# Optimization experiments

Measured on AMD Instinct MI355X. Metric: run time of the kernel, lower is better.

## Reference

```python
import jax, jax.numpy as jnp
import numpy as np

N = 8192
IN_F = 512
OUT_F = 64
NEG_INF = -9e15

def setup_inputs() -> dict:
    key = jax.random.key(0)
    k1, k2, k3, k4 = jax.random.split(key, 4)
    node_features = jax.random.normal(k1, (N, IN_F), dtype=jnp.float32)
    adjacency_matrix = jax.random.randint(k2, (N, N), 0, 2, dtype=jnp.int32)
    # Xavier-uniform-like init (gain 1.414), scale irrelevant for correctness
    w_bound = 1.414 * np.sqrt(6.0 / (IN_F + OUT_F))
    a_bound = 1.414 * np.sqrt(6.0 / (2 * OUT_F + 1))
    weight_matrix = jax.random.uniform(k3, (IN_F, OUT_F), minval=-w_bound, maxval=w_bound, dtype=jnp.float32)
    attention_vector = jax.random.uniform(k4, (2 * OUT_F, 1), minval=-a_bound, maxval=a_bound, dtype=jnp.float32)
    return {
        "node_features": node_features,
        "adjacency_matrix": adjacency_matrix,
        "weight_matrix": weight_matrix,
        "attention_vector": attention_vector,
    }

def reference(node_features, adjacency_matrix, weight_matrix, attention_vector):
    # h: [N, F] transformed features
    h = node_features @ weight_matrix
    # score[i, j] = h[i] . a_left + h[j] . a_right
    a_left = attention_vector[:OUT_F, 0]   # [F]
    a_right = attention_vector[OUT_F:, 0]  # [F]
    scores = (h @ a_left)[:, None] + (h @ a_right)[None, :]  # [N, N]
    # NOTE: source defines leaky_relu but never applies it in forward — faithful omission.
    masked = jnp.where(adjacency_matrix > 0, scores, NEG_INF)
    attn = jax.nn.softmax(masked, axis=1)  # [N, N]
    # dropout p=0 / inference: no-op
    out = attn @ h  # [N, F]
    return jax.nn.elu(out)  # concat=True path
```

## Files before the change

kernel.cpp:

```cpp
#include <hip/hip_runtime.h>
#include <hip/hip_bf16.h>
#include <cstdint>

#define NN      8192
#define OF      64
#define KC      16
#define CW      512
#define PSTR    65
#define RBYTES  1024

#define OFF_HW  0
#define OFF_P   1310720
#define OFF_BM  35389440

typedef __attribute__((ext_vector_type(8))) short  s16x8;
typedef __attribute__((ext_vector_type(4))) float  f32x4;

__device__ __forceinline__ unsigned short f2bf(float f) {
  unsigned int u = __float_as_uint(f);
  unsigned int r = (u + 0x7FFFu + ((u >> 16) & 1u)) >> 16;
  return (unsigned short)r;
}

__global__ __launch_bounds__(256) void ka_pack(const int* __restrict__ A,
                                               unsigned char* __restrict__ BM) {
  int t = threadIdx.x;
  int l = t & 63, w = t >> 6;
  int row = blockIdx.x * 4 + w;
  const int* ap = A + (size_t)row * NN + l * 8;
  unsigned char* bp = BM + (size_t)row * RBYTES + l;
#pragma unroll 4
  for (int i = 0; i < 16; ++i) {
    int4 a = *(const int4*)(ap + i * 512);
    int4 b = *(const int4*)(ap + i * 512 + 4);
    unsigned by = (unsigned)(a.x | (a.y << 1) | (a.z << 2) | (a.w << 3) |
                             (b.x << 4) | (b.y << 5) | (b.z << 6) | (b.w << 7));
    bp[i * 64] = (unsigned char)by;
  }
}

__global__ __launch_bounds__(256) void k1_hw(const float* __restrict__ X,
                                             const float* __restrict__ W,
                                             const float* __restrict__ att,
                                             unsigned short* __restrict__ HW) {
  __shared__ float xs[16 * 516];
  __shared__ float ws[64 * 68];
  int t = threadIdx.x;
  int rb = blockIdx.x * 16;

  {
    const float4* src = (const float4*)(X + (size_t)rb * 512);
#pragma unroll
    for (int s = 0; s < 8; ++s) {
      int lid = s * 256 + t;
      int row = lid >> 7, kseg = lid & 127;
      *(float4*)&xs[row * 516 + kseg * 4] = src[row * 128 + kseg];
    }
  }

  int row = t >> 4, tx = t & 15;
  float4 acc = {0.f, 0.f, 0.f, 0.f};
  for (int kc = 0; kc < 8; ++kc) {
    __syncthreads();
#pragma unroll
    for (int s = 0; s < 4; ++s) {
      int lid = s * 256 + t;
      int k = lid >> 4, cs = lid & 15;
      *(float4*)&ws[k * 68 + cs * 4] =
          *(const float4*)(W + (size_t)(kc * 64 + k) * 64 + cs * 4);
    }
    __syncthreads();
#pragma unroll 16
    for (int k = 0; k < 64; ++k) {
      float x = xs[row * 516 + kc * 64 + k];
      float4 w4 = *(const float4*)&ws[k * 68 + tx * 4];
      acc.x += x * w4.x; acc.y += x * w4.y;
      acc.z += x * w4.z; acc.w += x * w4.w;
    }
  }

  float v = acc.x * att[64 + tx * 4]     + acc.y * att[64 + tx * 4 + 1] +
            acc.z * att[64 + tx * 4 + 2] + acc.w * att[64 + tx * 4 + 3];
#pragma unroll
  for (int m = 8; m > 0; m >>= 1) v += __shfl_xor(v, m, 64);
  float e = expf(v);

  int j = rb + row;
  unsigned short* hw = HW + j;
  float hv[4] = {acc.x, acc.y, acc.z, acc.w};
#pragma unroll
  for (int c = 0; c < 4; ++c)
    hw[(size_t)(tx * 4 + c) * NN] = f2bf(e * hv[c]);
  if (tx == 0) hw[(size_t)64 * NN] = f2bf(e);
}

__device__ __forceinline__ s16x8 expand8(unsigned m) {
  union { unsigned u[4]; s16x8 v; } r;
#pragma unroll
  for (int j = 0; j < 4; ++j)
    r.u[j] = (((m >> (2 * j)) & 1u) | (((m >> (2 * j + 1)) & 1u) << 16)) * 0x3F80u;
  return r.v;
}

__device__ __forceinline__ unsigned u4c(uint4 v, int c) {
  return c == 0 ? v.x : c == 1 ? v.y : c == 2 ? v.z : v.w;
}

__global__ __launch_bounds__(256, 2) void k3_gat(const unsigned char* __restrict__ BM,
                                                 const unsigned short* __restrict__ HW,
                                                 float* __restrict__ P) {
  __shared__ unsigned short bt[65 * 512];

  int t = threadIdx.x;
  int kc = blockIdx.x & 15;
  int mg = blockIdx.x >> 4;
  int lane = t & 63, w = t >> 6;
  int l15 = lane & 15, q = lane >> 4;
  int k0 = kc * CW;
  int rowM = mg * 128;

  uint4 abits[2][4];
#pragma unroll
  for (int mt = 0; mt < 2; ++mt) {
    const uint4* p = (const uint4*)(BM +
        (size_t)(rowM + w * 32 + mt * 16 + l15) * RBYTES + kc * 64);
#pragma unroll
    for (int i = 0; i < 4; ++i) abits[mt][i] = p[i];
  }

#pragma unroll
  for (int rds = 0; rds < 16; ++rds) {
    int lid = rds * 256 + t;
    int row = lid >> 6, ch = lid & 63;
    uint4 v = *(const uint4*)(HW + (size_t)row * NN + k0 + ch * 8);
    *(uint4*)&bt[row * 512 + ((ch ^ (row & 7)) * 8)] = v;
  }
  if (t < 64) {
    uint4 v = *(const uint4*)(HW + (size_t)64 * NN + k0 + t * 8);
    *(uint4*)&bt[64 * 512 + t * 8] = v;
  }
  __syncthreads();

  int swz = l15 & 7;
  int bb[4][2];
#pragma unroll
  for (int tt = 0; tt < 4; ++tt)
#pragma unroll
    for (int ks = 0; ks < 2; ++ks)
      bb[tt][ks] = ((tt * 16 + l15) * 512 + (((ks * 4 + q) ^ swz) * 8)) * 2;
  int eb0 = (64 * 512 + q * 8) * 2;
  int eb1 = (64 * 512 + (4 + q) * 8) * 2;
  int qs = q * 8;

  f32x4 acc[2][5];
#pragma unroll
  for (int mt = 0; mt < 2; ++mt)
#pragma unroll
    for (int tt = 0; tt < 5; ++tt) acc[mt][tt] = 0.f;
  const s16x8 zero8 = {0, 0, 0, 0, 0, 0, 0, 0};

#pragma unroll
  for (int s = 0; s < 8; ++s) {
    s16x8 af[2][2];
#pragma unroll
    for (int mt = 0; mt < 2; ++mt) {
      unsigned d0 = u4c(abits[mt][s >> 1], 2 * (s & 1));
      unsigned d1 = u4c(abits[mt][s >> 1], 2 * (s & 1) + 1);
      af[mt][0] = expand8((d0 >> qs) & 0xFFu);
      af[mt][1] = expand8((d1 >> qs) & 0xFFu);
    }

    int so = s * 128;
#pragma unroll
    for (int ks = 0; ks < 2; ++ks) {
#pragma unroll
      for (int tt = 0; tt < 4; ++tt) {
        s16x8 b = *(const s16x8*)((char*)bt + bb[tt][ks] + so);
#pragma unroll
        for (int mt = 0; mt < 2; ++mt)
          acc[mt][tt] = __builtin_amdgcn_mfma_f32_16x16x32_bf16(af[mt][ks], b, acc[mt][tt], 0, 0, 0);
      }
      s16x8 b4 = *(const s16x8*)((char*)bt + (ks ? eb1 : eb0) + so);
      b4 = (l15 == 0) ? b4 : zero8;
#pragma unroll
      for (int mt = 0; mt < 2; ++mt)
        acc[mt][4] = __builtin_amdgcn_mfma_f32_16x16x32_bf16(af[mt][ks], b4, acc[mt][4], 0, 0, 0);
    }
  }

  float* Pp = P + (size_t)kc * NN * PSTR;
#pragma unroll
  for (int mt = 0; mt < 2; ++mt) {
    int rb = rowM + w * 32 + mt * 16 + q * 4;
#pragma unroll
    for (int tt = 0; tt < 4; ++tt)
#pragma unroll
      for (int rg = 0; rg < 4; ++rg)
        Pp[(size_t)(rb + rg) * PSTR + tt * 16 + l15] = acc[mt][tt][rg];
    if (l15 == 0)
#pragma unroll
      for (int rg = 0; rg < 4; ++rg)
        Pp[(size_t)(rb + rg) * PSTR + 64] = acc[mt][4][rg];
  }
}

__global__ __launch_bounds__(256) void k4_fin(const float* __restrict__ P,
                                              float* __restrict__ out) {
  int g = blockIdx.x * 256 + threadIdx.x;
  int i = g >> 6, c = g & 63;
  float num = 0.f, S = 0.f;
#pragma unroll
  for (int kc = 0; kc < KC; ++kc) {
    const float* p = P + (size_t)kc * NN * PSTR + (size_t)i * PSTR;
    num += p[c];
    S   += p[64];
  }
  float x = num / S;
  out[g] = x > 0.f ? x : expm1f(x);
}

extern "C" void kernel_launch(void* const* d_in, const int* in_sizes, int n_in,
                              void* d_out, int out_size, void* d_ws, size_t ws_size,
                              hipStream_t stream) {
  const float* X  = (const float*)d_in[0];
  const int*   A  = (const int*)d_in[1];
  const float* W  = (const float*)d_in[2];
  const float* av = (const float*)d_in[3];
  float* out = (float*)d_out;

  char* ws = (char*)d_ws;
  unsigned short* HW = (unsigned short*)(ws + OFF_HW);
  float*          P  = (float*)(ws + OFF_P);
  unsigned char*  BM = (unsigned char*)(ws + OFF_BM);

  ka_pack<<<NN / 4, 256, 0, stream>>>(A, BM);
  k1_hw<<<NN / 16, 256, 0, stream>>>(X, W, av, HW);
  k3_gat<<<64 * KC, 256, 0, stream>>>(BM, HW, P);
  k4_fin<<<(size_t)NN * OF / 256, 256, 0, stream>>>(P, out);
}
```

Measured before the change: 411.2 us.

## Pack adjacency bits via wave ballots and replace LDS swizzle with padded stride

The adjacency packing kernel now builds 64-bit masks with wavefront ballots over strided int4 loads instead of per-lane shift-or byte packing, which changes the bit layout of the packed mask. The GAT matmul kernel decodes the new layout by picking bits from four words per fragment. The LDS tile for HW drops the XOR swizzle in favour of a padded row stride of 520 elements to avoid bank conflicts. The aim is cheaper packing and fewer ALU ops per fragment, at the cost of a bit-mapping that must match exactly and a bit more LDS.

```diff
diff --git a/kernel.cpp b/kernel.cpp
--- a/kernel.cpp
+++ b/kernel.cpp
@@ -8,6 +8,7 @@
 #define CW      512
 #define PSTR    65
 #define RBYTES  1024
+#define BSTR    520
 
 #define OFF_HW  0
 #define OFF_P   1310720
@@ -23,19 +24,23 @@
 }
 
 __global__ __launch_bounds__(256) void ka_pack(const int* __restrict__ A,
-                                               unsigned char* __restrict__ BM) {
+                                               unsigned long long* __restrict__ BM) {
   int t = threadIdx.x;
   int l = t & 63, w = t >> 6;
   int row = blockIdx.x * 4 + w;
-  const int* ap = A + (size_t)row * NN + l * 8;
-  unsigned char* bp = BM + (size_t)row * RBYTES + l;
+  const int* ap = A + (size_t)row * NN + l * 4;
+  unsigned long long* bp = BM + (size_t)row * (RBYTES / 8);
 #pragma unroll 4
-  for (int i = 0; i < 16; ++i) {
-    int4 a = *(const int4*)(ap + i * 512);
-    int4 b = *(const int4*)(ap + i * 512 + 4);
-    unsigned by = (unsigned)(a.x | (a.y << 1) | (a.z << 2) | (a.w << 3) |
-                             (b.x << 4) | (b.y << 5) | (b.z << 6) | (b.w << 7));
-    bp[i * 64] = (unsigned char)by;
+  for (int g = 0; g < 32; ++g) {
+    int4 a = *(const int4*)(ap + g * 256);
+    unsigned long long b0 = __ballot(a.x != 0);
+    unsigned long long b1 = __ballot(a.y != 0);
+    unsigned long long b2 = __ballot(a.z != 0);
+    unsigned long long b3 = __ballot(a.w != 0);
+    if (l == 0) {
+      bp[g * 4 + 0] = b0; bp[g * 4 + 1] = b1;
+      bp[g * 4 + 2] = b2; bp[g * 4 + 3] = b3;
+    }
   }
 }
 
@@ -94,22 +99,17 @@
   if (tx == 0) hw[(size_t)64 * NN] = f2bf(e);
 }
 
-__device__ __forceinline__ s16x8 expand8(unsigned m) {
-  union { unsigned u[4]; s16x8 v; } r;
-#pragma unroll
-  for (int j = 0; j < 4; ++j)
-    r.u[j] = (((m >> (2 * j)) & 1u) | (((m >> (2 * j + 1)) & 1u) << 16)) * 0x3F80u;
-  return r.v;
-}
-
 __device__ __forceinline__ unsigned u4c(uint4 v, int c) {
   return c == 0 ? v.x : c == 1 ? v.y : c == 2 ? v.z : v.w;
+}
+__device__ __forceinline__ unsigned mk2(unsigned a, unsigned b) {
+  return ((a & 1u) | ((b & 1u) << 16)) * 0x3F80u;
 }
 
 __global__ __launch_bounds__(256, 2) void k3_gat(const unsigned char* __restrict__ BM,
                                                  const unsigned short* __restrict__ HW,
                                                  float* __restrict__ P) {
-  __shared__ unsigned short bt[65 * 512];
+  __shared__ unsigned short bt[65 * BSTR];
 
   int t = threadIdx.x;
   int kc = blockIdx.x & 15;
@@ -118,6 +118,7 @@
   int l15 = lane & 15, q = lane >> 4;
   int k0 = kc * CW;
   int rowM = mg * 128;
+  int q2 = q * 2;
 
   uint4 abits[2][4];
 #pragma unroll
@@ -133,24 +134,22 @@
     int lid = rds * 256 + t;
     int row = lid >> 6, ch = lid & 63;
     uint4 v = *(const uint4*)(HW + (size_t)row * NN + k0 + ch * 8);
-    *(uint4*)&bt[row * 512 + ((ch ^ (row & 7)) * 8)] = v;
+    *(uint4*)&bt[row * BSTR + ch * 8] = v;
   }
   if (t < 64) {
     uint4 v = *(const uint4*)(HW + (size_t)64 * NN + k0 + t * 8);
-    *(uint4*)&bt[64 * 512 + t * 8] = v;
+    *(uint4*)&bt[64 * BSTR + t * 8] = v;
   }
   __syncthreads();
 
-  int swz = l15 & 7;
   int bb[4][2];
 #pragma unroll
   for (int tt = 0; tt < 4; ++tt)
 #pragma unroll
     for (int ks = 0; ks < 2; ++ks)
-      bb[tt][ks] = ((tt * 16 + l15) * 512 + (((ks * 4 + q) ^ swz) * 8)) * 2;
-  int eb0 = (64 * 512 + q * 8) * 2;
-  int eb1 = (64 * 512 + (4 + q) * 8) * 2;
-  int qs = q * 8;
+      bb[tt][ks] = ((tt * 16 + l15) * BSTR + (ks * 4 + q) * 8) * 2;
+  int eb0 = (64 * BSTR + q * 8) * 2;
+  int eb1 = (64 * BSTR + (4 + q) * 8) * 2;
 
   f32x4 acc[2][5];
 #pragma unroll
@@ -161,13 +160,27 @@
 
 #pragma unroll
   for (int s = 0; s < 8; ++s) {
+    int base = (s >> 2) * 2;
+    int h = ((s & 3) >= 2) ? 1 : 0;
+    int bpc = (s & 1) * 16;
+
     s16x8 af[2][2];
 #pragma unroll
-    for (int mt = 0; mt < 2; ++mt) {
-      unsigned d0 = u4c(abits[mt][s >> 1], 2 * (s & 1));
-      unsigned d1 = u4c(abits[mt][s >> 1], 2 * (s & 1) + 1);
-      af[mt][0] = expand8((d0 >> qs) & 0xFFu);
-      af[mt][1] = expand8((d1 >> qs) & 0xFFu);
+    for (int ks = 0; ks < 2; ++ks) {
+      int sh = bpc + ks * 8;
+#pragma unroll
+      for (int mt = 0; mt < 2; ++mt) {
+        unsigned v0 = u4c(abits[mt][base],     0 + h) >> (sh + q2);
+        unsigned v1 = u4c(abits[mt][base],     2 + h) >> (sh + q2);
+        unsigned v2 = u4c(abits[mt][base + 1], 0 + h) >> (sh + q2);
+        unsigned v3 = u4c(abits[mt][base + 1], 2 + h) >> (sh + q2);
+        union { unsigned u[4]; s16x8 v; } fr;
+        fr.u[0] = mk2(v0, v1);
+        fr.u[1] = mk2(v2, v3);
+        fr.u[2] = mk2(v0 >> 1, v1 >> 1);
+        fr.u[3] = mk2(v2 >> 1, v3 >> 1);
+        af[mt][ks] = fr.v;
+      }
     }
 
     int so = s * 128;
@@ -229,12 +242,12 @@
   float* out = (float*)d_out;
 
   char* ws = (char*)d_ws;
-  unsigned short* HW = (unsigned short*)(ws + OFF_HW);
-  float*          P  = (float*)(ws + OFF_P);
-  unsigned char*  BM = (unsigned char*)(ws + OFF_BM);
+  unsigned short*     HW = (unsigned short*)(ws + OFF_HW);
+  float*              P  = (float*)(ws + OFF_P);
+  unsigned long long* BM = (unsigned long long*)(ws + OFF_BM);
 
   ka_pack<<<NN / 4, 256, 0, stream>>>(A, BM);
   k1_hw<<<NN / 16, 256, 0, stream>>>(X, W, av, HW);
-  k3_gat<<<64 * KC, 256, 0, stream>>>(BM, HW, P);
+  k3_gat<<<64 * KC, 256, 0, stream>>>((const unsigned char*)BM, HW, P);
   k4_fin<<<(size_t)NN * OF / 256, 256, 0, stream>>>(P, out);
 }
```

Result: no change. 416.0 us (+1.2%).
